# Kernel optimization log

Hardware: AMD Instinct MI355X
Metric: run time of the kernel (lower is better)

The kernel has to match this reference:

```python
import jax, jax.numpy as jnp
import numpy as np

BS, V, H, W = 2, 4, 24, 24
C, K, L, NH = 256, 16, 6, 8
DH = C // NH
FF = 4 * C
EPS = 1e-5


def _ln(x, w, b):
    m = jnp.mean(x, axis=-1, keepdims=True)
    v = jnp.mean((x - m) ** 2, axis=-1, keepdims=True)
    return (x - m) * jax.lax.rsqrt(v + EPS) * w + b


def _pe(x, W1, b1, W2, b2):
    # PositionEmbeddingLearnedMLP: Linear(3,C) -> ReLU -> Linear(C,C), channels-last
    return jax.nn.relu(x @ W1.T + b1) @ W2.T + b2


def setup_inputs():
    key = jax.random.key(0)
    ks = jax.random.split(key, 8)
    s = 0.02
    return {
        "feature": jax.random.normal(ks[0], (BS * V, C, H, W), jnp.float32),
        "xyz": jax.random.uniform(ks[1], (BS * V, H, W, 3), jnp.float32),
        "pe_W1": jax.random.normal(ks[2], (C, 3), jnp.float32) * s,
        "pe_b1": jnp.zeros((C,), jnp.float32),
        "pe_W2": jax.random.normal(ks[3], (C, C), jnp.float32) * s,
        "pe_b2": jnp.zeros((C,), jnp.float32),
        "Wqkv": jax.random.normal(ks[4], (L, 3 * C, C), jnp.float32) * s,
        "bqkv": jnp.zeros((L, 3 * C), jnp.float32),
        "Wo": jax.random.normal(ks[5], (L, C, C), jnp.float32) * s,
        "bo": jnp.zeros((L, C), jnp.float32),
        "ln_attn_w": jnp.ones((L, C), jnp.float32),
        "ln_attn_b": jnp.zeros((L, C), jnp.float32),
        "W1": jax.random.normal(ks[6], (L, FF, C), jnp.float32) * s,
        "b1": jnp.zeros((L, FF), jnp.float32),
        "W2": jax.random.normal(ks[7], (L, C, FF), jnp.float32) * s,
        "b2": jnp.zeros((L, C), jnp.float32),
        "ln_ffn_w": jnp.ones((L, C), jnp.float32),
        "ln_ffn_b": jnp.zeros((L, C), jnp.float32),
        "ln_out_w": jnp.ones((L, C), jnp.float32),
        "ln_out_b": jnp.zeros((L, C), jnp.float32),
    }


def _forward(feature, xyz, pe_W1, pe_b1, pe_W2, pe_b2, Wqkv, bqkv, Wo, bo,
             ln_attn_w, ln_attn_b, W1, b1, W2, b2, ln_ffn_w, ln_ffn_b,
             ln_out_w, ln_out_b):
    N = V * H * W
    # (B*V,C,H,W) -> (BS,N,C) ; (B*V,H,W,3) -> (BS,N,3) : flatten views+pixels
    feat = feature.reshape(BS, V, C, H, W).transpose(0, 1, 3, 4, 2).reshape(BS, N, C)
    pts = xyz.reshape(BS, N, 3)
    # per-batch KNN (self included), mirroring pointops.queryandgroup
    d2 = jnp.sum((pts[:, :, None, :] - pts[:, None, :, :]) ** 2, axis=-1)  # (BS,N,N)
    _, idx = jax.lax.top_k(-d2, K)  # (BS,N,K) nearest-neighbor indices
    grouped = jax.vmap(lambda p, i: p[i])(pts, idx)  # (BS,N,K,3)
    rel = grouped - pts[:, :, None, :]  # relative coords (use_xyz=True)
    q_pe = _pe(jnp.zeros((3,), feat.dtype), pe_W1, pe_b1, pe_W2, pe_b2)  # (C,)
    k_pe = _pe(rel, pe_W1, pe_b1, pe_W2, pe_b2).reshape(BS * N, K, C)
    idx_g = (idx + (jnp.arange(BS) * N)[:, None, None]).reshape(BS * N, K)
    out = feat.reshape(BS * N, C)
    for i in range(L):
        keyf = out[idx_g]  # (BN,K,C) per-layer neighbor gather
        # CrossAttentionLayer, pre-norm
        t2 = _ln(out, ln_attn_w[i], ln_attn_b[i])
        q = (t2 + q_pe) @ Wqkv[i, :C].T + bqkv[i, :C]
        k = (keyf + k_pe) @ Wqkv[i, C:2 * C].T + bqkv[i, C:2 * C]
        v = keyf @ Wqkv[i, 2 * C:].T + bqkv[i, 2 * C:]
        qh = q.reshape(-1, NH, DH)
        kh = k.reshape(-1, K, NH, DH)
        vh = v.reshape(-1, K, NH, DH)
        att = jax.nn.softmax(jnp.einsum('bhd,bkhd->bhk', qh, kh) * (DH ** -0.5), axis=-1)
        ao = jnp.einsum('bhk,bkhd->bhd', att, vh).reshape(-1, C) @ Wo[i].T + bo[i]
        out = out + ao
        # FFNLayer, pre-norm
        t2 = _ln(out, ln_ffn_w[i], ln_ffn_b[i])
        out = out + (jax.nn.relu(t2 @ W1[i].T + b1[i]) @ W2[i].T + b2[i])
        # extra per-layer LayerNorm
        out = _ln(out, ln_out_w[i], ln_out_b[i])
    return out.reshape(BS, V, H, W, C).transpose(0, 1, 4, 2, 3).reshape(BS * V, C, H, W)


def reference(feature, xyz, pe_W1, pe_b1, pe_W2, pe_b2, Wqkv, bqkv, Wo, bo,
              ln_attn_w, ln_attn_b, W1, b1, W2, b2, ln_ffn_w, ln_ffn_b,
              ln_out_w, ln_out_b):
    return _forward(feature, xyz, pe_W1, pe_b1, pe_W2, pe_b2, Wqkv, bqkv, Wo, bo,
                    ln_attn_w, ln_attn_b, W1, b1, W2, b2, ln_ffn_w, ln_ffn_b,
                    ln_out_w, ln_out_b)
```

## Files before the change

### kernel.cpp

```cpp
#include <hip/hip_runtime.h>
#include <math.h>

#define BS_ 2
#define V_ 4
#define H_ 24
#define W_ 24
#define N_ (V_*H_*W_)
#define BN_ (BS_*N_)
#define C_ 256
#define K_ 16
#define L_ 6
#define NH_ 8
#define DH_ 32
#define FF_ 1024

typedef __attribute__((ext_vector_type(4))) float f32x4;
typedef __attribute__((ext_vector_type(8))) short bf16x8;
typedef __attribute__((ext_vector_type(4))) unsigned u32x4;

__device__ inline unsigned short f2bf(float x) {
    unsigned u = __float_as_uint(x);
    unsigned r = u + 0x7fffu + ((u >> 16) & 1u);
    return (unsigned short)(r >> 16);
}
__device__ inline float bf2f(unsigned short h) {
    return __uint_as_float(((unsigned)h) << 16);
}

__global__ __launch_bounds__(256) void f2bf5_kernel(const float* __restrict__ s0,
                                                    const float* __restrict__ s1,
                                                    const float* __restrict__ s2,
                                                    const float* __restrict__ s3,
                                                    const float* __restrict__ s4,
                                                    unsigned short* __restrict__ dst) {
    const int c0 = 65536, c1 = 1245184, c2 = 1638400, c3 = 3211264, c4 = 4784128;
    int i = blockIdx.x*256 + threadIdx.x;
    if (i >= c4) return;
    float v;
    if (i < c0)      v = s0[i];
    else if (i < c1) v = s1[i - c0];
    else if (i < c2) v = s2[i - c1];
    else if (i < c3) v = s3[i - c2];
    else             v = s4[i - c3];
    dst[i] = f2bf(v);
}

__global__ __launch_bounds__(256) void reshape_in_ln(const float* __restrict__ f,
                                                     const float* __restrict__ lnw,
                                                     const float* __restrict__ lnb,
                                                     const float* __restrict__ qpe,
                                                     float* __restrict__ w_out,
                                                     unsigned short* __restrict__ b_out,
                                                     unsigned short* __restrict__ b_t2) {
    int bn = blockIdx.x, c = threadIdx.x;
    int b = bn / N_, rem = bn % N_;
    int v = rem / (H_*W_), hw = rem % (H_*W_);
    float x = f[(((size_t)(b*V_ + v)*C_ + c)*(H_*W_)) + hw];
    w_out[(size_t)bn*C_ + c] = x;
    b_out[(size_t)bn*C_ + c] = f2bf(x);
    __shared__ float red[4];
    float s = x;
    #pragma unroll
    for (int off = 32; off; off >>= 1) s += __shfl_xor(s, off, 64);
    if ((c & 63) == 0) red[c >> 6] = s;
    __syncthreads();
    float mean = (red[0]+red[1]+red[2]+red[3]) * (1.f/C_);
    __syncthreads();
    float dx = x - mean;
    s = dx*dx;
    #pragma unroll
    for (int off = 32; off; off >>= 1) s += __shfl_xor(s, off, 64);
    if ((c & 63) == 0) red[c >> 6] = s;
    __syncthreads();
    float var = (red[0]+red[1]+red[2]+red[3]) * (1.f/C_);
    float y = dx * rsqrtf(var + 1e-5f) * lnw[c] + lnb[c] + qpe[c];
    b_t2[(size_t)bn*C_ + c] = f2bf(y);
}

__global__ __launch_bounds__(256) void reshape_out_kernel(const float* __restrict__ in,
                                                          float* __restrict__ o) {
    int bn = blockIdx.x, c = threadIdx.x;
    int b = bn / N_, rem = bn % N_;
    int v = rem / (H_*W_), hw = rem % (H_*W_);
    o[(((size_t)(b*V_ + v)*C_ + c)*(H_*W_)) + hw] = in[(size_t)bn*C_ + c];
}

__global__ __launch_bounds__(256) void knn_kernel(const float* __restrict__ pts,
                                                  int* __restrict__ idx) {
    int wid = threadIdx.x >> 6, lane = threadIdx.x & 63;
    int point = blockIdx.x*4 + wid;
    int b = point / N_;
    int il = point % N_;
    __shared__ float ps[N_*3];
    for (int l = threadIdx.x; l < N_*3; l += 256) ps[l] = pts[(size_t)b*N_*3 + l];
    __syncthreads();
    float qx = ps[il*3], qy = ps[il*3+1], qz = ps[il*3+2];
    unsigned long long key[36];
    #pragma unroll
    for (int s = 0; s < 36; ++s) {
        int j = lane + 64*s;
        float dx = qx - ps[j*3], dy = qy - ps[j*3+1], dz = qz - ps[j*3+2];
        float d2 = dx*dx + dy*dy + dz*dz;
        key[s] = ((unsigned long long)__float_as_uint(d2) << 32) | (unsigned)j;
    }
    for (int it = 0; it < K_; ++it) {
        unsigned long long b0 = key[0], b1 = key[1], b2 = key[2], b3 = key[3];
        #pragma unroll
        for (int s = 4; s < 36; s += 4) {
            b0 = key[s]   < b0 ? key[s]   : b0;
            b1 = key[s+1] < b1 ? key[s+1] : b1;
            b2 = key[s+2] < b2 ? key[s+2] : b2;
            b3 = key[s+3] < b3 ? key[s+3] : b3;
        }
        unsigned long long m01 = b0 < b1 ? b0 : b1;
        unsigned long long m23 = b2 < b3 ? b2 : b3;
        unsigned long long best = m01 < m23 ? m01 : m23;
        #pragma unroll
        for (int off = 32; off; off >>= 1) {
            unsigned long long o = __shfl_xor(best, off, 64);
            if (o < best) best = o;
        }
        int wj = (int)(best & 0xffffffffu);
        if (lane == 0) idx[point*K_ + it] = b*N_ + wj;
        if ((wj & 63) == lane) {
            int sw = wj >> 6;
            #pragma unroll
            for (int s = 0; s < 36; ++s) if (s == sw) key[s] = ~0ull;
        }
    }
}

__global__ __launch_bounds__(256) void qpe_kernel(const float* __restrict__ b1,
                                                  const float* __restrict__ W2,
                                                  const float* __restrict__ b2,
                                                  float* __restrict__ qpe) {
    __shared__ float h[C_];
    int tid = threadIdx.x;
    h[tid] = fmaxf(b1[tid], 0.f);
    __syncthreads();
    float acc = 0.f;
    for (int j = 0; j < C_; ++j) acc += h[j] * W2[(size_t)tid*C_ + j];
    qpe[tid] = acc + b2[tid];
}

__global__ __launch_bounds__(256) void kpe_kernel(const float* __restrict__ pts,
                                                  const int* __restrict__ idx,
                                                  const float* __restrict__ W1,
                                                  const float* __restrict__ b1,
                                                  const unsigned short* __restrict__ Wpe,
                                                  const float* __restrict__ pb2,
                                                  unsigned short* __restrict__ kpe) {
    int tid = threadIdx.x;
    int wave = tid >> 6, lane = tid & 63;
    int wr = wave >> 1, wc = wave & 1;
    int n0 = blockIdx.x * 64;
    int m0 = blockIdx.y * 64;
    __shared__ float relS[64][4];
    __shared__ float w1S[256][4];
    __shared__ unsigned short hid[64][264];
    __shared__ unsigned short Ws[2][64][40];
    w1S[tid][0] = W1[tid*3+0];
    w1S[tid][1] = W1[tid*3+1];
    w1S[tid][2] = W1[tid*3+2];
    w1S[tid][3] = b1[tid];
    if (tid < 64) {
        int row = m0 + tid;
        int p = row >> 4;
        int j = idx[row];
        relS[tid][0] = pts[(size_t)j*3+0] - pts[(size_t)p*3+0];
        relS[tid][1] = pts[(size_t)j*3+1] - pts[(size_t)p*3+1];
        relS[tid][2] = pts[(size_t)j*3+2] - pts[(size_t)p*3+2];
    }
    int rw = tid >> 2, ch = tid & 3;
    const unsigned short* pW = Wpe + (size_t)(n0 + rw)*C_ + ch*8;
    *(bf16x8*)&Ws[0][rw][ch*8] = *(const bf16x8*)pW;
    __syncthreads();
    {
        int r = tid >> 2, cq = (tid & 3) * 64;
        float r0 = relS[r][0], r1 = relS[r][1], r2 = relS[r][2];
        #pragma unroll
        for (int u8 = 0; u8 < 8; ++u8) {
            unsigned short tmp[8];
            #pragma unroll
            for (int v = 0; v < 8; ++v) {
                int c = cq + u8*8 + v;
                f32x4 w4 = *(const f32x4*)&w1S[c][0];
                float val = r0*w4[0] + r1*w4[1] + r2*w4[2] + w4[3];
                tmp[v] = f2bf(fmaxf(val, 0.f));
            }
            *(bf16x8*)&hid[r][cq + u8*8] = *(bf16x8*)tmp;
        }
    }
    __syncthreads();
    f32x4 acc[2][2];
    #pragma unroll
    for (int i = 0; i < 2; ++i)
        #pragma unroll
        for (int j = 0; j < 2; ++j) acc[i][j] = (f32x4){0.f,0.f,0.f,0.f};
    for (int t = 0; t < 8; ++t) {
        int cur = t & 1;
        bool nx = (t < 7);
        bf16x8 lw;
        if (nx) lw = *(const bf16x8*)(pW + (t+1)*32);
        int kf = (lane >> 4) * 8;
        bf16x8 af[2], wf[2];
        #pragma unroll
        for (int i = 0; i < 2; ++i) af[i] = *(const bf16x8*)&hid[wr*32 + i*16 + (lane & 15)][t*32 + kf];
        #pragma unroll
        for (int j = 0; j < 2; ++j) wf[j] = *(const bf16x8*)&Ws[cur][wc*32 + j*16 + (lane & 15)][kf];
        #pragma unroll
        for (int i = 0; i < 2; ++i)
            #pragma unroll
            for (int j = 0; j < 2; ++j)
                acc[i][j] = __builtin_amdgcn_mfma_f32_16x16x32_bf16(af[i], wf[j], acc[i][j], 0, 0, 0);
        if (nx) *(bf16x8*)&Ws[cur^1][rw][ch*8] = lw;
        __syncthreads();
    }
    #pragma unroll
    for (int i = 0; i < 2; ++i)
        #pragma unroll
        for (int j = 0; j < 2; ++j)
            #pragma unroll
            for (int rg = 0; rg < 4; ++rg) {
                int mr = m0 + wr*32 + i*16 + (lane >> 4)*4 + rg;
                int col = n0 + wc*32 + j*16 + (lane & 15);
                kpe[(size_t)mr*C_ + col] = f2bf(acc[i][j][rg] + pb2[col]);
            }
}

template<int ACT, bool RES, int OMODE>
__device__ __forceinline__ void gemm_body(const unsigned short* __restrict__ A, int sA,
                                          const unsigned short* __restrict__ W, int sW,
                                          const float* __restrict__ bias, int bcol0,
                                          const float* __restrict__ res,
                                          float* __restrict__ outF,
                                          unsigned short* __restrict__ outB,
                                          int sO, int on0, int m0, int K) {
    __shared__ unsigned short As[2][64][40];
    __shared__ unsigned short Ws[2][64][40];
    int tid = threadIdx.x;
    int wave = tid >> 6, lane = tid & 63;
    int wr = wave >> 1, wc = wave & 1;
    f32x4 acc[2][2];
    #pragma unroll
    for (int i = 0; i < 2; ++i)
        #pragma unroll
        for (int j = 0; j < 2; ++j) acc[i][j] = (f32x4){0.f, 0.f, 0.f, 0.f};

    int r = tid >> 2, ch = tid & 3;
    const unsigned short* pA = A + (size_t)(m0 + r)*sA + ch*8;
    const unsigned short* pW = W + (size_t)r*sW + ch*8;
    *(bf16x8*)&As[0][r][ch*8] = *(const bf16x8*)pA;
    *(bf16x8*)&Ws[0][r][ch*8] = *(const bf16x8*)pW;
    __syncthreads();
    int nk = K >> 5;
    for (int t = 0; t < nk; ++t) {
        int cur = t & 1;
        bool has_next = (t + 1 < nk);
        bf16x8 la, lw;
        if (has_next) {
            la = *(const bf16x8*)(pA + (t+1)*32);
            lw = *(const bf16x8*)(pW + (t+1)*32);
        }
        int kf = (lane >> 4) * 8;
        bf16x8 af[2], wf[2];
        #pragma unroll
        for (int i = 0; i < 2; ++i) af[i] = *(const bf16x8*)&As[cur][wr*32 + i*16 + (lane & 15)][kf];
        #pragma unroll
        for (int j = 0; j < 2; ++j) wf[j] = *(const bf16x8*)&Ws[cur][wc*32 + j*16 + (lane & 15)][kf];
        #pragma unroll
        for (int i = 0; i < 2; ++i)
            #pragma unroll
            for (int j = 0; j < 2; ++j)
                acc[i][j] = __builtin_amdgcn_mfma_f32_16x16x32_bf16(af[i], wf[j], acc[i][j], 0, 0, 0);
        if (has_next) {
            *(bf16x8*)&As[cur^1][r][ch*8] = la;
            *(bf16x8*)&Ws[cur^1][r][ch*8] = lw;
        }
        __syncthreads();
    }
    #pragma unroll
    for (int i = 0; i < 2; ++i) {
        #pragma unroll
        for (int j = 0; j < 2; ++j) {
            #pragma unroll
            for (int rg = 0; rg < 4; ++rg) {
                int m = m0 + wr*32 + i*16 + (lane >> 4)*4 + rg;
                int pl = wc*32 + j*16 + (lane & 15);
                float v = acc[i][j][rg];
                if (bias) v += bias[bcol0 + pl];
                if (ACT == 1) v = fmaxf(v, 0.f);
                if (RES) v += res[(size_t)m*sO + on0 + pl];
                if (OMODE != 2) outF[(size_t)m*sO + on0 + pl] = v;
                if (OMODE != 0) outB[(size_t)m*sO + on0 + pl] = f2bf(v);
            }
        }
    }
}

template<int ACT, bool RES, int OMODE>
__global__ __launch_bounds__(256) void gemm_k(const unsigned short* __restrict__ A,
                                              const unsigned short* __restrict__ W,
                                              const float* __restrict__ bias,
                                              const float* __restrict__ res,
                                              float* __restrict__ outF,
                                              unsigned short* __restrict__ outB,
                                              int P, int K) {
    int n0 = blockIdx.x * 64, m0 = blockIdx.y * 64;
    gemm_body<ACT,RES,OMODE>(A, K, W + (size_t)n0*K, K, bias, n0, res, outF, outB, P, n0, m0, K);
}

__global__ __launch_bounds__(256) void qkv_kernel(const unsigned short* __restrict__ t2,
                                                  const unsigned short* __restrict__ outb,
                                                  const unsigned short* __restrict__ Wqkv_l,
                                                  const float* __restrict__ bqkv_l,
                                                  unsigned short* __restrict__ b_q,
                                                  unsigned short* __restrict__ b_kv) {
    int bx = blockIdx.x;
    int n0 = bx * 64;
    int m0 = blockIdx.y * 64;
    if (bx < 4) {
        gemm_body<0,false,2>(t2, C_, Wqkv_l + (size_t)n0*C_, C_, bqkv_l, n0,
                             nullptr, nullptr, b_q, 256, n0, m0, C_);
    } else {
        gemm_body<0,false,2>(outb, C_, Wqkv_l + (size_t)n0*C_, C_, bqkv_l, n0,
                             nullptr, nullptr, b_kv, 512, n0 - 256, m0, C_);
    }
}

template<int VAR>
__global__ __launch_bounds__(256) void gemm_ln(const unsigned short* __restrict__ A,
                                               const unsigned short* __restrict__ W,
                                               const float* __restrict__ bias,
                                               const float* __restrict__ res,
                                               const float* __restrict__ lnw1, const float* __restrict__ lnb1,
                                               const float* __restrict__ lnw2, const float* __restrict__ lnb2,
                                               const float* __restrict__ qpe,
                                               float* __restrict__ outF,
                                               unsigned short* __restrict__ outB,
                                               unsigned short* __restrict__ outT2,
                                               int K) {
    __shared__ unsigned short Ws[2][256][40];
    __shared__ unsigned short As[2][16][40];
    int tid = threadIdx.x;
    int wave = tid >> 6, lane = tid & 63;
    int m0 = blockIdx.x * 16;
    f32x4 acc[4];
    #pragma unroll
    for (int j = 0; j < 4; ++j) acc[j] = (f32x4){0.f,0.f,0.f,0.f};
    int rw = tid >> 2, ch = tid & 3;
    const unsigned short* pW = W + (size_t)rw*K + ch*8;
    const unsigned short* pA = A + (size_t)(m0 + ((tid & 63) >> 2))*K + (tid & 3)*8;
    #pragma unroll
    for (int c = 0; c < 4; ++c)
        *(bf16x8*)&Ws[0][c*64 + rw][ch*8] = *(const bf16x8*)(pW + (size_t)c*64*K);
    if (tid < 64) *(bf16x8*)&As[0][tid >> 2][(tid & 3)*8] = *(const bf16x8*)pA;
    __syncthreads();
    int nk = K >> 5;
    for (int t = 0; t < nk; ++t) {
        int cur = t & 1;
        bool nx = (t + 1 < nk);
        bf16x8 lw0, lw1, lw2, lw3, la;
        if (nx) {
            lw0 = *(const bf16x8*)(pW + (size_t)0*64*K + (t+1)*32);
            lw1 = *(const bf16x8*)(pW + (size_t)1*64*K + (t+1)*32);
            lw2 = *(const bf16x8*)(pW + (size_t)2*64*K + (t+1)*32);
            lw3 = *(const bf16x8*)(pW + (size_t)3*64*K + (t+1)*32);
            if (tid < 64) la = *(const bf16x8*)(pA + (t+1)*32);
        }
        int kf = (lane >> 4) * 8;
        bf16x8 af = *(const bf16x8*)&As[cur][lane & 15][kf];
        #pragma unroll
        for (int j = 0; j < 4; ++j) {
            bf16x8 wf = *(const bf16x8*)&Ws[cur][wave*64 + j*16 + (lane & 15)][kf];
            acc[j] = __builtin_amdgcn_mfma_f32_16x16x32_bf16(af, wf, acc[j], 0, 0, 0);
        }
        if (nx) {
            *(bf16x8*)&Ws[cur^1][0*64 + rw][ch*8] = lw0;
            *(bf16x8*)&Ws[cur^1][1*64 + rw][ch*8] = lw1;
            *(bf16x8*)&Ws[cur^1][2*64 + rw][ch*8] = lw2;
            *(bf16x8*)&Ws[cur^1][3*64 + rw][ch*8] = lw3;
            if (tid < 64) *(bf16x8*)&As[cur^1][tid >> 2][(tid & 3)*8] = la;
        }
        __syncthreads();
    }
    float* S = (float*)&Ws[0][0][0];
    #pragma unroll
    for (int j = 0; j < 4; ++j) {
        int col = wave*64 + j*16 + (lane & 15);
        #pragma unroll
        for (int rg = 0; rg < 4; ++rg) {
            int row = (lane >> 4)*4 + rg;
            S[row*260 + col] = acc[j][rg] + bias[col] + res[(size_t)(m0+row)*C_ + col];
        }
    }
    __syncthreads();
    int row = tid >> 4, g = tid & 15;
    size_t m = m0 + row;
    float x[16];
    #pragma unroll
    for (int u = 0; u < 4; ++u) {
        f32x4 v4 = *(const f32x4*)&S[row*260 + g*16 + u*4];
        x[u*4+0] = v4[0]; x[u*4+1] = v4[1]; x[u*4+2] = v4[2]; x[u*4+3] = v4[3];
    }
    float s1 = 0.f, s2 = 0.f;
    #pragma unroll
    for (int u = 0; u < 16; ++u) { s1 += x[u]; s2 += x[u]*x[u]; }
    #pragma unroll
    for (int off = 8; off; off >>= 1) { s1 += __shfl_xor(s1, off, 16); s2 += __shfl_xor(s2, off, 16); }
    float mean = s1 * (1.f/C_);
    float var  = s2 * (1.f/C_) - mean*mean;
    float rstd = rsqrtf(var + 1e-5f);
    float y1[16];
    #pragma unroll
    for (int u = 0; u < 4; ++u) {
        f32x4 w4 = *(const f32x4*)&lnw1[g*16 + u*4];
        f32x4 b4 = *(const f32x4*)&lnb1[g*16 + u*4];
        #pragma unroll
        for (int v = 0; v < 4; ++v)
            y1[u*4+v] = (x[u*4+v] - mean)*rstd*w4[v] + b4[v];
    }
    if (VAR == 0) {
        #pragma unroll
        for (int u = 0; u < 4; ++u) {
            f32x4 v4 = { x[u*4], x[u*4+1], x[u*4+2], x[u*4+3] };
            *(f32x4*)&outF[m*C_ + g*16 + u*4] = v4;
        }
        unsigned pk[8];
        #pragma unroll
        for (int u = 0; u < 8; ++u) pk[u] = (unsigned)f2bf(y1[2*u]) | ((unsigned)f2bf(y1[2*u+1]) << 16);
        *(u32x4*)&outT2[m*C_ + g*16]     = *(u32x4*)&pk[0];
        *(u32x4*)&outT2[m*C_ + g*16 + 8] = *(u32x4*)&pk[4];
    } else {
        #pragma unroll
        for (int u = 0; u < 4; ++u) {
            f32x4 v4 = { y1[u*4], y1[u*4+1], y1[u*4+2], y1[u*4+3] };
            *(f32x4*)&outF[m*C_ + g*16 + u*4] = v4;
        }
        if (VAR == 1) {
            unsigned pk[8];
            #pragma unroll
            for (int u = 0; u < 8; ++u) pk[u] = (unsigned)f2bf(y1[2*u]) | ((unsigned)f2bf(y1[2*u+1]) << 16);
            *(u32x4*)&outB[m*C_ + g*16]     = *(u32x4*)&pk[0];
            *(u32x4*)&outB[m*C_ + g*16 + 8] = *(u32x4*)&pk[4];
            float t1 = 0.f, t2s = 0.f;
            #pragma unroll
            for (int u = 0; u < 16; ++u) { t1 += y1[u]; t2s += y1[u]*y1[u]; }
            #pragma unroll
            for (int off = 8; off; off >>= 1) { t1 += __shfl_xor(t1, off, 16); t2s += __shfl_xor(t2s, off, 16); }
            float mean2 = t1 * (1.f/C_);
            float var2  = t2s * (1.f/C_) - mean2*mean2;
            float rstd2 = rsqrtf(var2 + 1e-5f);
            unsigned pk2[8];
            #pragma unroll
            for (int u = 0; u < 4; ++u) {
                f32x4 w4 = *(const f32x4*)&lnw2[g*16 + u*4];
                f32x4 b4 = *(const f32x4*)&lnb2[g*16 + u*4];
                f32x4 q4 = *(const f32x4*)&qpe[g*16 + u*4];
                float z0 = (y1[u*4+0]-mean2)*rstd2*w4[0] + b4[0] + q4[0];
                float z1 = (y1[u*4+1]-mean2)*rstd2*w4[1] + b4[1] + q4[1];
                float z2 = (y1[u*4+2]-mean2)*rstd2*w4[2] + b4[2] + q4[2];
                float z3 = (y1[u*4+3]-mean2)*rstd2*w4[3] + b4[3] + q4[3];
                pk2[u*2]   = (unsigned)f2bf(z0) | ((unsigned)f2bf(z1) << 16);
                pk2[u*2+1] = (unsigned)f2bf(z2) | ((unsigned)f2bf(z3) << 16);
            }
            *(u32x4*)&outT2[m*C_ + g*16]     = *(u32x4*)&pk2[0];
            *(u32x4*)&outT2[m*C_ + g*16 + 8] = *(u32x4*)&pk2[4];
        }
    }
}

__global__ __launch_bounds__(256) void rk_kernel(const unsigned short* __restrict__ q,
                                                 const unsigned short* __restrict__ Wqkv_l,
                                                 unsigned short* __restrict__ r) {
    int n0 = blockIdx.x * 64, m0 = blockIdx.y * 64, h = blockIdx.z;
    __shared__ unsigned short As[64][40];
    __shared__ unsigned short Ws[64][40];
    int tid = threadIdx.x;
    int wave = tid >> 6, lane = tid & 63;
    int wr = wave >> 1, wc = wave & 1;
    *(bf16x8*)&As[tid>>2][(tid&3)*8] =
        *(const bf16x8*)&q[(size_t)(m0 + (tid>>2))*C_ + h*DH_ + (tid&3)*8];
    {
        int d = tid >> 3, cg = tid & 7;
        bf16x8 wv = *(const bf16x8*)&Wqkv_l[(size_t)(C_ + h*DH_ + d)*C_ + n0 + cg*8];
        #pragma unroll
        for (int j = 0; j < 8; ++j) Ws[cg*8 + j][d] = (unsigned short)wv[j];
    }
    __syncthreads();
    int kf = (lane >> 4) * 8;
    bf16x8 af[2], wf[2];
    #pragma unroll
    for (int i = 0; i < 2; ++i) af[i] = *(const bf16x8*)&As[wr*32 + i*16 + (lane & 15)][kf];
    #pragma unroll
    for (int j = 0; j < 2; ++j) wf[j] = *(const bf16x8*)&Ws[wc*32 + j*16 + (lane & 15)][kf];
    f32x4 acc[2][2];
    #pragma unroll
    for (int i = 0; i < 2; ++i)
        #pragma unroll
        for (int j = 0; j < 2; ++j)
            acc[i][j] = __builtin_amdgcn_mfma_f32_16x16x32_bf16(af[i], wf[j],
                          (f32x4){0.f,0.f,0.f,0.f}, 0, 0, 0);
    #pragma unroll
    for (int i = 0; i < 2; ++i)
        #pragma unroll
        for (int j = 0; j < 2; ++j)
            #pragma unroll
            for (int rg = 0; rg < 4; ++rg) {
                int m = m0 + wr*32 + i*16 + (lane >> 4)*4 + rg;
                int pl = wc*32 + j*16 + (lane & 15);
                r[(size_t)m*(NH_*C_) + h*C_ + n0 + pl] = f2bf(acc[i][j][rg]);
            }
}

__global__ __launch_bounds__(256) void attn_kernel(const unsigned short* __restrict__ q,
                                                   const unsigned short* __restrict__ kv,
                                                   const unsigned short* __restrict__ kpe,
                                                   const unsigned short* __restrict__ r,
                                                   const int* __restrict__ idx,
                                                   unsigned short* __restrict__ ao) {
    int wid = threadIdx.x >> 6, lane = threadIdx.x & 63;
    int point = blockIdx.x*4 + wid;
    __shared__ __align__(16) unsigned short vs[4][K_][264];
    __shared__ __align__(16) float atts[4][NH_][K_];
    int row = lane & 15;
    int off8 = (lane >> 4) * 8;
    int idx_l = idx[point*K_ + row];

    #pragma unroll
    for (int t = 0; t < 8; ++t) {
        int vr = 2*t + (lane >> 5);
        int j = __shfl(idx_l, vr, 64);
        int cc = (lane & 31) * 8;
        *(bf16x8*)&vs[wid][vr][cc] = *(const bf16x8*)&kv[(size_t)j*512 + 256 + cc];
    }

    f32x4 acc = {0.f, 0.f, 0.f, 0.f};
    const bf16x8 zero8 = {0,0,0,0,0,0,0,0};
    #pragma unroll
    for (int s = 0; s < 8; ++s) {
        bf16x8 a = *(const bf16x8*)&kpe[((size_t)point*K_ + row)*C_ + s*32 + off8];
        bf16x8 b = zero8;
        if (row < 8) b = *(const bf16x8*)&r[(size_t)point*NH_*C_ + row*C_ + s*32 + off8];
        acc = __builtin_amdgcn_mfma_f32_16x16x32_bf16(a, b, acc, 0, 0, 0);
    }
    #pragma unroll
    for (int s = 0; s < 8; ++s) {
        bf16x8 a = *(const bf16x8*)&kv[(size_t)idx_l*512 + s*32 + off8];
        bf16x8 b = zero8;
        if (row == 8 + s) b = *(const bf16x8*)&q[(size_t)point*C_ + s*32 + off8];
        acc = __builtin_amdgcn_mfma_f32_16x16x32_bf16(a, b, acc, 0, 0, 0);
    }

    const float scale = 0.1767766952966369f;
    float sv[4], m = -1e30f;
    #pragma unroll
    for (int rg = 0; rg < 4; ++rg) {
        float o = __shfl_xor(acc[rg], 8, 64);
        sv[rg] = (acc[rg] + o) * scale;
        m = fmaxf(m, sv[rg]);
    }
    m = fmaxf(m, __shfl_xor(m, 16, 64));
    m = fmaxf(m, __shfl_xor(m, 32, 64));
    float sum = 0.f;
    #pragma unroll
    for (int rg = 0; rg < 4; ++rg) { sv[rg] = __expf(sv[rg] - m); sum += sv[rg]; }
    sum += __shfl_xor(sum, 16, 64);
    sum += __shfl_xor(sum, 32, 64);
    float inv = 1.f / sum;
    if (row < 8) {
        f32x4 av = { sv[0]*inv, sv[1]*inv, sv[2]*inv, sv[3]*inv };
        *(f32x4*)&atts[wid][row][(lane >> 4) * 4] = av;
    }

    int h = lane >> 3;
    float att_f[16];
    #pragma unroll
    for (int u = 0; u < 4; ++u) {
        f32x4 t4 = *(const f32x4*)&atts[wid][h][u*4];
        att_f[u*4+0] = t4[0]; att_f[u*4+1] = t4[1]; att_f[u*4+2] = t4[2]; att_f[u*4+3] = t4[3];
    }
    int cbase = lane * 4;
    float o0 = 0.f, o1 = 0.f, o2 = 0.f, o3 = 0.f;
    #pragma unroll
    for (int k = 0; k < K_; ++k) {
        unsigned long long vv = *(const unsigned long long*)&vs[wid][k][cbase];
        unsigned lo = (unsigned)vv, hi = (unsigned)(vv >> 32);
        float a = att_f[k];
        o0 += a * __uint_as_float(lo << 16);
        o1 += a * __uint_as_float(lo & 0xffff0000u);
        o2 += a * __uint_as_float(hi << 16);
        o3 += a * __uint_as_float(hi & 0xffff0000u);
    }
    unsigned p0 = (unsigned)f2bf(o0) | ((unsigned)f2bf(o1) << 16);
    unsigned p1 = (unsigned)f2bf(o2) | ((unsigned)f2bf(o3) << 16);
    unsigned out2[2] = { p0, p1 };
    *(unsigned long long*)&ao[(size_t)point*C_ + cbase] = *(const unsigned long long*)out2;
}

extern "C" void kernel_launch(void* const* d_in, const int* in_sizes, int n_in,
                              void* d_out, int out_size, void* d_ws, size_t ws_size,
                              hipStream_t stream) {
    const float* feature  = (const float*)d_in[0];
    const float* xyz      = (const float*)d_in[1];
    const float* pe_W1    = (const float*)d_in[2];
    const float* pe_b1    = (const float*)d_in[3];
    const float* pe_W2    = (const float*)d_in[4];
    const float* pe_b2    = (const float*)d_in[5];
    const float* Wqkv     = (const float*)d_in[6];
    const float* bqkv     = (const float*)d_in[7];
    const float* Wo       = (const float*)d_in[8];
    const float* bo       = (const float*)d_in[9];
    const float* ln_attn_w= (const float*)d_in[10];
    const float* ln_attn_b= (const float*)d_in[11];
    const float* W1       = (const float*)d_in[12];
    const float* b1       = (const float*)d_in[13];
    const float* W2       = (const float*)d_in[14];
    const float* b2       = (const float*)d_in[15];
    const float* ln_ffn_w = (const float*)d_in[16];
    const float* ln_ffn_b = (const float*)d_in[17];
    const float* ln_out_w = (const float*)d_in[18];
    const float* ln_out_b = (const float*)d_in[19];

    float* ws = (float*)d_ws;
    float* w_out = ws;
    float* w_qpe = w_out + (size_t)BN_*C_;
    unsigned short* bptr = (unsigned short*)(w_qpe + C_ + 64);
    unsigned short* b_out = bptr;  bptr += (size_t)BN_*C_;
    unsigned short* b_t2  = bptr;  bptr += (size_t)BN_*C_;
    unsigned short* b_q   = bptr;  bptr += (size_t)BN_*C_;
    unsigned short* b_kv  = bptr;  bptr += (size_t)BN_*512;
    unsigned short* b_ao  = bptr;  bptr += (size_t)BN_*C_;
    unsigned short* b_ffh = bptr;  bptr += (size_t)BN_*FF_;
    unsigned short* w_kpe = bptr;  bptr += (size_t)BN_*K_*C_;
    unsigned short* w_r   = bptr;  bptr += (size_t)BN_*NH_*C_;
    unsigned short* bWpe  = bptr;  bptr += (size_t)C_*C_;
    unsigned short* bWqkv = bptr;  bptr += (size_t)L_*3*C_*C_;
    unsigned short* bWo   = bptr;  bptr += (size_t)L_*C_*C_;
    unsigned short* bW1   = bptr;  bptr += (size_t)L_*FF_*C_;
    unsigned short* bW2   = bptr;  bptr += (size_t)L_*C_*FF_;
    int* w_idx = (int*)bptr;

    f2bf5_kernel<<<(4784128 + 255)/256, 256, 0, stream>>>(pe_W2, Wqkv, Wo, W1, W2, bWpe);
    knn_kernel<<<BN_/4, 256, 0, stream>>>(xyz, w_idx);
    qpe_kernel<<<1, 256, 0, stream>>>(pe_b1, pe_W2, pe_b2, w_qpe);
    reshape_in_ln<<<BN_, 256, 0, stream>>>(feature, ln_attn_w, ln_attn_b, w_qpe,
                                           w_out, b_out, b_t2);
    kpe_kernel<<<dim3(C_/64, (BN_*K_)/64), 256, 0, stream>>>(xyz, w_idx, pe_W1, pe_b1,
                                                             bWpe, pe_b2, w_kpe);

    for (int i = 0; i < L_; ++i) {
        const unsigned short* Wqkv_l = bWqkv + (size_t)i*3*C_*C_;
        const float* bqkv_l = bqkv + (size_t)i*3*C_;

        qkv_kernel<<<dim3(12, BN_/64), 256, 0, stream>>>(b_t2, b_out, Wqkv_l, bqkv_l, b_q, b_kv);
        rk_kernel<<<dim3(4, BN_/64, NH_), 256, 0, stream>>>(b_q, Wqkv_l, w_r);
        attn_kernel<<<BN_/4, 256, 0, stream>>>(b_q, b_kv, w_kpe, w_r, w_idx, b_ao);
        gemm_ln<0><<<BN_/16, 256, 0, stream>>>(
            b_ao, bWo + (size_t)i*C_*C_, bo + i*C_, w_out,
            ln_ffn_w + i*C_, ln_ffn_b + i*C_, nullptr, nullptr, nullptr,
            w_out, nullptr, b_t2, C_);
        gemm_k<1,false,2><<<dim3(FF_/64, BN_/64), 256, 0, stream>>>(
            b_t2, bW1 + (size_t)i*FF_*C_, b1 + i*FF_, nullptr, nullptr, b_ffh, FF_, C_);
        if (i < L_-1) {
            gemm_ln<1><<<BN_/16, 256, 0, stream>>>(
                b_ffh, bW2 + (size_t)i*C_*FF_, b2 + i*C_, w_out,
                ln_out_w + i*C_, ln_out_b + i*C_,
                ln_attn_w + (i+1)*C_, ln_attn_b + (i+1)*C_, w_qpe,
                w_out, b_out, b_t2, FF_);
        } else {
            gemm_ln<2><<<BN_/16, 256, 0, stream>>>(
                b_ffh, bW2 + (size_t)i*C_*FF_, b2 + i*C_, w_out,
                ln_out_w + i*C_, ln_out_b + i*C_, nullptr, nullptr, nullptr,
                w_out, nullptr, nullptr, FF_);
        }
    }

    reshape_out_kernel<<<BN_, 256, 0, stream>>>(w_out, (float*)d_out);
}
```

Measured before the change: 682.6 us.

## Pre-swizzle weights into MFMA fragment layout and load B operands directly to registers

Adds a weight conversion kernel that writes bf16 weights in per-lane MFMA fragment order, so the GEMM kernels load B fragments straight from global memory into registers instead of staging them through shared memory. Both the tiled GEMM and the GEMM+LayerNorm kernels drop their weight LDS buffers and the matching stores. The key positional-embedding kernel is split into a hidden-layer kernel that writes a large bf16 intermediate plus a generic GEMM. The trade-offs are extra conversion launches each call, an extra global round trip for the PE hidden activations, and a plain bf16 copy of Wqkv still kept for rk_kernel.

```diff
diff --git a/kernel.cpp b/kernel.cpp
--- a/kernel.cpp
+++ b/kernel.cpp
@@ -27,22 +27,24 @@
     return __uint_as_float(((unsigned)h) << 16);
 }
 
-__global__ __launch_bounds__(256) void f2bf5_kernel(const float* __restrict__ s0,
-                                                    const float* __restrict__ s1,
-                                                    const float* __restrict__ s2,
-                                                    const float* __restrict__ s3,
-                                                    const float* __restrict__ s4,
-                                                    unsigned short* __restrict__ dst) {
-    const int c0 = 65536, c1 = 1245184, c2 = 1638400, c3 = 3211264, c4 = 4784128;
+__global__ __launch_bounds__(256) void f2bf_kernel(const float* __restrict__ in,
+                                                   unsigned short* __restrict__ out, int n) {
     int i = blockIdx.x*256 + threadIdx.x;
-    if (i >= c4) return;
-    float v;
-    if (i < c0)      v = s0[i];
-    else if (i < c1) v = s1[i - c0];
-    else if (i < c2) v = s2[i - c1];
-    else if (i < c3) v = s3[i - c2];
-    else             v = s4[i - c3];
-    dst[i] = f2bf(v);
+    if (i < n) out[i] = f2bf(in[i]);
+}
+
+__global__ __launch_bounds__(256) void w2frag_kernel(const float* __restrict__ W,
+                                                     unsigned short* __restrict__ F,
+                                                     int P, int K) {
+    int wid = threadIdx.x >> 6, lane = threadIdx.x & 63;
+    int tile = blockIdx.x*4 + wid;
+    int nkt = K >> 5;
+    int tn = tile / nkt, tk = tile - tn*nkt;
+    const float* src = W + (size_t)(tn*16 + (lane & 15))*K + tk*32 + (lane >> 4)*8;
+    unsigned short tmp[8];
+    #pragma unroll
+    for (int j = 0; j < 8; ++j) tmp[j] = f2bf(src[j]);
+    *(bf16x8*)&F[(size_t)tile*512 + lane*8] = *(bf16x8*)tmp;
 }
 
 __global__ __launch_bounds__(256) void reshape_in_ln(const float* __restrict__ f,
@@ -143,104 +145,41 @@
     qpe[tid] = acc + b2[tid];
 }
 
-__global__ __launch_bounds__(256) void kpe_kernel(const float* __restrict__ pts,
-                                                  const int* __restrict__ idx,
-                                                  const float* __restrict__ W1,
-                                                  const float* __restrict__ b1,
-                                                  const unsigned short* __restrict__ Wpe,
-                                                  const float* __restrict__ pb2,
-                                                  unsigned short* __restrict__ kpe) {
+__global__ __launch_bounds__(256) void pe_hidden_kernel(const float* __restrict__ pts,
+                                                        const int* __restrict__ idx,
+                                                        const float* __restrict__ W1,
+                                                        const float* __restrict__ b1,
+                                                        unsigned short* __restrict__ hidden) {
+    int point = blockIdx.x;
+    int c = threadIdx.x;
+    __shared__ float rel[K_][3];
+    if (threadIdx.x < K_*3) {
+        int k = threadIdx.x / 3, ax = threadIdx.x % 3;
+        int j = idx[point*K_ + k];
+        rel[k][ax] = pts[(size_t)j*3 + ax] - pts[(size_t)point*3 + ax];
+    }
+    __syncthreads();
+    float w0 = W1[c*3], w1 = W1[c*3+1], w2 = W1[c*3+2], bb = b1[c];
+    #pragma unroll
+    for (int k = 0; k < K_; ++k) {
+        float v = rel[k][0]*w0 + rel[k][1]*w1 + rel[k][2]*w2 + bb;
+        hidden[((size_t)point*K_ + k)*C_ + c] = f2bf(fmaxf(v, 0.f));
+    }
+}
+
+template<int ACT, bool RES, int OMODE>
+__device__ __forceinline__ void gemm_body2(const unsigned short* __restrict__ A, int sA,
+                                           const unsigned short* __restrict__ Wf,
+                                           const float* __restrict__ bias, int bcol0,
+                                           const float* __restrict__ res,
+                                           float* __restrict__ outF,
+                                           unsigned short* __restrict__ outB,
+                                           int sO, int on0, int m0, int K) {
+    __shared__ unsigned short As[2][64][40];
     int tid = threadIdx.x;
     int wave = tid >> 6, lane = tid & 63;
     int wr = wave >> 1, wc = wave & 1;
-    int n0 = blockIdx.x * 64;
-    int m0 = blockIdx.y * 64;
-    __shared__ float relS[64][4];
-    __shared__ float w1S[256][4];
-    __shared__ unsigned short hid[64][264];
-    __shared__ unsigned short Ws[2][64][40];
-    w1S[tid][0] = W1[tid*3+0];
-    w1S[tid][1] = W1[tid*3+1];
-    w1S[tid][2] = W1[tid*3+2];
-    w1S[tid][3] = b1[tid];
-    if (tid < 64) {
-        int row = m0 + tid;
-        int p = row >> 4;
-        int j = idx[row];
-        relS[tid][0] = pts[(size_t)j*3+0] - pts[(size_t)p*3+0];
-        relS[tid][1] = pts[(size_t)j*3+1] - pts[(size_t)p*3+1];
-        relS[tid][2] = pts[(size_t)j*3+2] - pts[(size_t)p*3+2];
-    }
-    int rw = tid >> 2, ch = tid & 3;
-    const unsigned short* pW = Wpe + (size_t)(n0 + rw)*C_ + ch*8;
-    *(bf16x8*)&Ws[0][rw][ch*8] = *(const bf16x8*)pW;
-    __syncthreads();
-    {
-        int r = tid >> 2, cq = (tid & 3) * 64;
-        float r0 = relS[r][0], r1 = relS[r][1], r2 = relS[r][2];
-        #pragma unroll
-        for (int u8 = 0; u8 < 8; ++u8) {
-            unsigned short tmp[8];
-            #pragma unroll
-            for (int v = 0; v < 8; ++v) {
-                int c = cq + u8*8 + v;
-                f32x4 w4 = *(const f32x4*)&w1S[c][0];
-                float val = r0*w4[0] + r1*w4[1] + r2*w4[2] + w4[3];
-                tmp[v] = f2bf(fmaxf(val, 0.f));
-            }
-            *(bf16x8*)&hid[r][cq + u8*8] = *(bf16x8*)tmp;
-        }
-    }
-    __syncthreads();
-    f32x4 acc[2][2];
-    #pragma unroll
-    for (int i = 0; i < 2; ++i)
-        #pragma unroll
-        for (int j = 0; j < 2; ++j) acc[i][j] = (f32x4){0.f,0.f,0.f,0.f};
-    for (int t = 0; t < 8; ++t) {
-        int cur = t & 1;
-        bool nx = (t < 7);
-        bf16x8 lw;
-        if (nx) lw = *(const bf16x8*)(pW + (t+1)*32);
-        int kf = (lane >> 4) * 8;
-        bf16x8 af[2], wf[2];
-        #pragma unroll
-        for (int i = 0; i < 2; ++i) af[i] = *(const bf16x8*)&hid[wr*32 + i*16 + (lane & 15)][t*32 + kf];
-        #pragma unroll
-        for (int j = 0; j < 2; ++j) wf[j] = *(const bf16x8*)&Ws[cur][wc*32 + j*16 + (lane & 15)][kf];
-        #pragma unroll
-        for (int i = 0; i < 2; ++i)
-            #pragma unroll
-            for (int j = 0; j < 2; ++j)
-                acc[i][j] = __builtin_amdgcn_mfma_f32_16x16x32_bf16(af[i], wf[j], acc[i][j], 0, 0, 0);
-        if (nx) *(bf16x8*)&Ws[cur^1][rw][ch*8] = lw;
-        __syncthreads();
-    }
-    #pragma unroll
-    for (int i = 0; i < 2; ++i)
-        #pragma unroll
-        for (int j = 0; j < 2; ++j)
-            #pragma unroll
-            for (int rg = 0; rg < 4; ++rg) {
-                int mr = m0 + wr*32 + i*16 + (lane >> 4)*4 + rg;
-                int col = n0 + wc*32 + j*16 + (lane & 15);
-                kpe[(size_t)mr*C_ + col] = f2bf(acc[i][j][rg] + pb2[col]);
-            }
-}
-
-template<int ACT, bool RES, int OMODE>
-__device__ __forceinline__ void gemm_body(const unsigned short* __restrict__ A, int sA,
-                                          const unsigned short* __restrict__ W, int sW,
-                                          const float* __restrict__ bias, int bcol0,
-                                          const float* __restrict__ res,
-                                          float* __restrict__ outF,
-                                          unsigned short* __restrict__ outB,
-                                          int sO, int on0, int m0, int K) {
-    __shared__ unsigned short As[2][64][40];
-    __shared__ unsigned short Ws[2][64][40];
-    int tid = threadIdx.x;
-    int wave = tid >> 6, lane = tid & 63;
-    int wr = wave >> 1, wc = wave & 1;
+    int nkt = K >> 5;
     f32x4 acc[2][2];
     #pragma unroll
     for (int i = 0; i < 2; ++i)
@@ -249,34 +188,29 @@
 
     int r = tid >> 2, ch = tid & 3;
     const unsigned short* pA = A + (size_t)(m0 + r)*sA + ch*8;
-    const unsigned short* pW = W + (size_t)r*sW + ch*8;
+    const unsigned short* bb = Wf + (size_t)(wc*2)*nkt*512 + lane*8;
     *(bf16x8*)&As[0][r][ch*8] = *(const bf16x8*)pA;
-    *(bf16x8*)&Ws[0][r][ch*8] = *(const bf16x8*)pW;
-    __syncthreads();
-    int nk = K >> 5;
-    for (int t = 0; t < nk; ++t) {
+    bf16x8 bw0 = *(const bf16x8*)bb;
+    bf16x8 bw1 = *(const bf16x8*)(bb + (size_t)nkt*512);
+    __syncthreads();
+    for (int t = 0; t < nkt; ++t) {
         int cur = t & 1;
-        bool has_next = (t + 1 < nk);
-        bf16x8 la, lw;
-        if (has_next) {
-            la = *(const bf16x8*)(pA + (t+1)*32);
-            lw = *(const bf16x8*)(pW + (t+1)*32);
+        bool nx = (t + 1 < nkt);
+        bf16x8 la, nb0, nb1;
+        if (nx) {
+            la  = *(const bf16x8*)(pA + (t+1)*32);
+            nb0 = *(const bf16x8*)(bb + (size_t)(t+1)*512);
+            nb1 = *(const bf16x8*)(bb + (size_t)nkt*512 + (size_t)(t+1)*512);
         }
         int kf = (lane >> 4) * 8;
-        bf16x8 af[2], wf[2];
-        #pragma unroll
-        for (int i = 0; i < 2; ++i) af[i] = *(const bf16x8*)&As[cur][wr*32 + i*16 + (lane & 15)][kf];
-        #pragma unroll
-        for (int j = 0; j < 2; ++j) wf[j] = *(const bf16x8*)&Ws[cur][wc*32 + j*16 + (lane & 15)][kf];
-        #pragma unroll
-        for (int i = 0; i < 2; ++i)
-            #pragma unroll
-            for (int j = 0; j < 2; ++j)
-                acc[i][j] = __builtin_amdgcn_mfma_f32_16x16x32_bf16(af[i], wf[j], acc[i][j], 0, 0, 0);
-        if (has_next) {
-            *(bf16x8*)&As[cur^1][r][ch*8] = la;
-            *(bf16x8*)&Ws[cur^1][r][ch*8] = lw;
-        }
+        bf16x8 af0 = *(const bf16x8*)&As[cur][wr*32 + (lane & 15)][kf];
+        bf16x8 af1 = *(const bf16x8*)&As[cur][wr*32 + 16 + (lane & 15)][kf];
+        acc[0][0] = __builtin_amdgcn_mfma_f32_16x16x32_bf16(af0, bw0, acc[0][0], 0, 0, 0);
+        acc[0][1] = __builtin_amdgcn_mfma_f32_16x16x32_bf16(af0, bw1, acc[0][1], 0, 0, 0);
+        acc[1][0] = __builtin_amdgcn_mfma_f32_16x16x32_bf16(af1, bw0, acc[1][0], 0, 0, 0);
+        acc[1][1] = __builtin_amdgcn_mfma_f32_16x16x32_bf16(af1, bw1, acc[1][1], 0, 0, 0);
+        if (nx) *(bf16x8*)&As[cur^1][r][ch*8] = la;
+        bw0 = nb0; bw1 = nb1;
         __syncthreads();
     }
     #pragma unroll
@@ -299,99 +233,92 @@
 }
 
 template<int ACT, bool RES, int OMODE>
-__global__ __launch_bounds__(256) void gemm_k(const unsigned short* __restrict__ A,
-                                              const unsigned short* __restrict__ W,
-                                              const float* __restrict__ bias,
-                                              const float* __restrict__ res,
-                                              float* __restrict__ outF,
-                                              unsigned short* __restrict__ outB,
-                                              int P, int K) {
-    int n0 = blockIdx.x * 64, m0 = blockIdx.y * 64;
-    gemm_body<ACT,RES,OMODE>(A, K, W + (size_t)n0*K, K, bias, n0, res, outF, outB, P, n0, m0, K);
-}
-
-__global__ __launch_bounds__(256) void qkv_kernel(const unsigned short* __restrict__ t2,
-                                                  const unsigned short* __restrict__ outb,
-                                                  const unsigned short* __restrict__ Wqkv_l,
-                                                  const float* __restrict__ bqkv_l,
-                                                  unsigned short* __restrict__ b_q,
-                                                  unsigned short* __restrict__ b_kv) {
-    int bx = blockIdx.x;
-    int n0 = bx * 64;
-    int m0 = blockIdx.y * 64;
-    if (bx < 4) {
-        gemm_body<0,false,2>(t2, C_, Wqkv_l + (size_t)n0*C_, C_, bqkv_l, n0,
-                             nullptr, nullptr, b_q, 256, n0, m0, C_);
-    } else {
-        gemm_body<0,false,2>(outb, C_, Wqkv_l + (size_t)n0*C_, C_, bqkv_l, n0,
-                             nullptr, nullptr, b_kv, 512, n0 - 256, m0, C_);
-    }
-}
-
-template<int VAR>
-__global__ __launch_bounds__(256) void gemm_ln(const unsigned short* __restrict__ A,
-                                               const unsigned short* __restrict__ W,
+__global__ __launch_bounds__(256) void gemm_k2(const unsigned short* __restrict__ A,
+                                               const unsigned short* __restrict__ Wf0,
                                                const float* __restrict__ bias,
                                                const float* __restrict__ res,
-                                               const float* __restrict__ lnw1, const float* __restrict__ lnb1,
-                                               const float* __restrict__ lnw2, const float* __restrict__ lnb2,
-                                               const float* __restrict__ qpe,
                                                float* __restrict__ outF,
                                                unsigned short* __restrict__ outB,
-                                               unsigned short* __restrict__ outT2,
-                                               int K) {
-    __shared__ unsigned short Ws[2][256][40];
+                                               int P, int K) {
+    int n0 = blockIdx.x * 64, m0 = blockIdx.y * 64;
+    const unsigned short* Wf = Wf0 + (size_t)(n0 >> 4)*(K >> 5)*512;
+    gemm_body2<ACT,RES,OMODE>(A, K, Wf, bias, n0, res, outF, outB, P, n0, m0, K);
+}
+
+__global__ __launch_bounds__(256) void qkv_kernel2(const unsigned short* __restrict__ t2,
+                                                   const unsigned short* __restrict__ outb,
+                                                   const unsigned short* __restrict__ Fqkv_l,
+                                                   const float* __restrict__ bqkv_l,
+                                                   unsigned short* __restrict__ b_q,
+                                                   unsigned short* __restrict__ b_kv) {
+    int bx = blockIdx.x;
+    int m0 = blockIdx.y * 64;
+    const unsigned short* Wf = Fqkv_l + (size_t)(bx*4)*8*512;
+    if (bx < 4) {
+        gemm_body2<0,false,2>(t2, C_, Wf, bqkv_l, bx*64, nullptr, nullptr, b_q, 256, bx*64, m0, C_);
+    } else {
+        gemm_body2<0,false,2>(outb, C_, Wf, bqkv_l, bx*64, nullptr, nullptr, b_kv, 512, bx*64 - 256, m0, C_);
+    }
+}
+
+template<int VAR>
+__global__ __launch_bounds__(256) void gemm_ln2(const unsigned short* __restrict__ A,
+                                                const unsigned short* __restrict__ Wf,
+                                                const float* __restrict__ bias,
+                                                const float* __restrict__ res,
+                                                const float* __restrict__ lnw1, const float* __restrict__ lnb1,
+                                                const float* __restrict__ lnw2, const float* __restrict__ lnb2,
+                                                const float* __restrict__ qpe,
+                                                float* __restrict__ outF,
+                                                unsigned short* __restrict__ outB,
+                                                unsigned short* __restrict__ outT2,
+                                                int K) {
     __shared__ unsigned short As[2][16][40];
+    __shared__ float S[16][260];
     int tid = threadIdx.x;
     int wave = tid >> 6, lane = tid & 63;
     int m0 = blockIdx.x * 16;
+    int nkt = K >> 5;
     f32x4 acc[4];
     #pragma unroll
     for (int j = 0; j < 4; ++j) acc[j] = (f32x4){0.f,0.f,0.f,0.f};
-    int rw = tid >> 2, ch = tid & 3;
-    const unsigned short* pW = W + (size_t)rw*K + ch*8;
     const unsigned short* pA = A + (size_t)(m0 + ((tid & 63) >> 2))*K + (tid & 3)*8;
-    #pragma unroll
-    for (int c = 0; c < 4; ++c)
-        *(bf16x8*)&Ws[0][c*64 + rw][ch*8] = *(const bf16x8*)(pW + (size_t)c*64*K);
+    const unsigned short* bb = Wf + (size_t)(wave*4)*nkt*512 + lane*8;
     if (tid < 64) *(bf16x8*)&As[0][tid >> 2][(tid & 3)*8] = *(const bf16x8*)pA;
-    __syncthreads();
-    int nk = K >> 5;
-    for (int t = 0; t < nk; ++t) {
+    bf16x8 bw[4];
+    #pragma unroll
+    for (int j = 0; j < 4; ++j) bw[j] = *(const bf16x8*)(bb + (size_t)j*nkt*512);
+    __syncthreads();
+    for (int t = 0; t < nkt; ++t) {
         int cur = t & 1;
-        bool nx = (t + 1 < nk);
-        bf16x8 lw0, lw1, lw2, lw3, la;
+        bool nx = (t + 1 < nkt);
+        bf16x8 la, nb0, nb1, nb2, nb3;
         if (nx) {
-            lw0 = *(const bf16x8*)(pW + (size_t)0*64*K + (t+1)*32);
-            lw1 = *(const bf16x8*)(pW + (size_t)1*64*K + (t+1)*32);
-            lw2 = *(const bf16x8*)(pW + (size_t)2*64*K + (t+1)*32);
-            lw3 = *(const bf16x8*)(pW + (size_t)3*64*K + (t+1)*32);
+            nb0 = *(const bf16x8*)(bb + (size_t)0*nkt*512 + (size_t)(t+1)*512);
+            nb1 = *(const bf16x8*)(bb + (size_t)1*nkt*512 + (size_t)(t+1)*512);
+            nb2 = *(const bf16x8*)(bb + (size_t)2*nkt*512 + (size_t)(t+1)*512);
+            nb3 = *(const bf16x8*)(bb + (size_t)3*nkt*512 + (size_t)(t+1)*512);
             if (tid < 64) la = *(const bf16x8*)(pA + (t+1)*32);
         }
         int kf = (lane >> 4) * 8;
         bf16x8 af = *(const bf16x8*)&As[cur][lane & 15][kf];
-        #pragma unroll
-        for (int j = 0; j < 4; ++j) {
-            bf16x8 wf = *(const bf16x8*)&Ws[cur][wave*64 + j*16 + (lane & 15)][kf];
-            acc[j] = __builtin_amdgcn_mfma_f32_16x16x32_bf16(af, wf, acc[j], 0, 0, 0);
-        }
+        acc[0] = __builtin_amdgcn_mfma_f32_16x16x32_bf16(af, bw[0], acc[0], 0, 0, 0);
+        acc[1] = __builtin_amdgcn_mfma_f32_16x16x32_bf16(af, bw[1], acc[1], 0, 0, 0);
+        acc[2] = __builtin_amdgcn_mfma_f32_16x16x32_bf16(af, bw[2], acc[2], 0, 0, 0);
+        acc[3] = __builtin_amdgcn_mfma_f32_16x16x32_bf16(af, bw[3], acc[3], 0, 0, 0);
         if (nx) {
-            *(bf16x8*)&Ws[cur^1][0*64 + rw][ch*8] = lw0;
-            *(bf16x8*)&Ws[cur^1][1*64 + rw][ch*8] = lw1;
-            *(bf16x8*)&Ws[cur^1][2*64 + rw][ch*8] = lw2;
-            *(bf16x8*)&Ws[cur^1][3*64 + rw][ch*8] = lw3;
             if (tid < 64) *(bf16x8*)&As[cur^1][tid >> 2][(tid & 3)*8] = la;
+            bw[0] = nb0; bw[1] = nb1; bw[2] = nb2; bw[3] = nb3;
         }
         __syncthreads();
     }
-    float* S = (float*)&Ws[0][0][0];
     #pragma unroll
     for (int j = 0; j < 4; ++j) {
         int col = wave*64 + j*16 + (lane & 15);
         #pragma unroll
         for (int rg = 0; rg < 4; ++rg) {
             int row = (lane >> 4)*4 + rg;
-            S[row*260 + col] = acc[j][rg] + bias[col] + res[(size_t)(m0+row)*C_ + col];
+            S[row][col] = acc[j][rg] + bias[col] + res[(size_t)(m0+row)*C_ + col];
         }
     }
     __syncthreads();
@@ -400,7 +327,7 @@
     float x[16];
     #pragma unroll
     for (int u = 0; u < 4; ++u) {
-        f32x4 v4 = *(const f32x4*)&S[row*260 + g*16 + u*4];
+        f32x4 v4 = *(const f32x4*)&S[row][g*16 + u*4];
         x[u*4+0] = v4[0]; x[u*4+1] = v4[1]; x[u*4+2] = v4[2]; x[u*4+3] = v4[3];
     }
     float s1 = 0.f, s2 = 0.f;
@@ -634,43 +561,52 @@
     unsigned short* b_ffh = bptr;  bptr += (size_t)BN_*FF_;
     unsigned short* w_kpe = bptr;  bptr += (size_t)BN_*K_*C_;
     unsigned short* w_r   = bptr;  bptr += (size_t)BN_*NH_*C_;
-    unsigned short* bWpe  = bptr;  bptr += (size_t)C_*C_;
+    unsigned short* b_hid = bptr;  bptr += (size_t)BN_*K_*C_;
     unsigned short* bWqkv = bptr;  bptr += (size_t)L_*3*C_*C_;
-    unsigned short* bWo   = bptr;  bptr += (size_t)L_*C_*C_;
-    unsigned short* bW1   = bptr;  bptr += (size_t)L_*FF_*C_;
-    unsigned short* bW2   = bptr;  bptr += (size_t)L_*C_*FF_;
+    unsigned short* Fqkv  = bptr;  bptr += (size_t)L_*3*C_*C_;
+    unsigned short* Fo    = bptr;  bptr += (size_t)L_*C_*C_;
+    unsigned short* F1    = bptr;  bptr += (size_t)L_*FF_*C_;
+    unsigned short* F2    = bptr;  bptr += (size_t)L_*C_*FF_;
+    unsigned short* Fpe   = bptr;  bptr += (size_t)C_*C_;
     int* w_idx = (int*)bptr;
 
-    f2bf5_kernel<<<(4784128 + 255)/256, 256, 0, stream>>>(pe_W2, Wqkv, Wo, W1, W2, bWpe);
+    f2bf_kernel<<<(L_*3*C_*C_+255)/256, 256, 0, stream>>>(Wqkv, bWqkv, L_*3*C_*C_);
+    w2frag_kernel<<<(L_*3*C_*C_/512)/4, 256, 0, stream>>>(Wqkv, Fqkv, L_*3*C_, C_);
+    w2frag_kernel<<<(L_*C_*C_/512)/4,   256, 0, stream>>>(Wo,   Fo,   L_*C_,   C_);
+    w2frag_kernel<<<(L_*FF_*C_/512)/4,  256, 0, stream>>>(W1,   F1,   L_*FF_,  C_);
+    w2frag_kernel<<<(L_*C_*FF_/512)/4,  256, 0, stream>>>(W2,   F2,   L_*C_,   FF_);
+    w2frag_kernel<<<(C_*C_/512)/4,      256, 0, stream>>>(pe_W2, Fpe, C_,      C_);
+
     knn_kernel<<<BN_/4, 256, 0, stream>>>(xyz, w_idx);
     qpe_kernel<<<1, 256, 0, stream>>>(pe_b1, pe_W2, pe_b2, w_qpe);
     reshape_in_ln<<<BN_, 256, 0, stream>>>(feature, ln_attn_w, ln_attn_b, w_qpe,
                                            w_out, b_out, b_t2);
-    kpe_kernel<<<dim3(C_/64, (BN_*K_)/64), 256, 0, stream>>>(xyz, w_idx, pe_W1, pe_b1,
-                                                             bWpe, pe_b2, w_kpe);
+    pe_hidden_kernel<<<BN_, 256, 0, stream>>>(xyz, w_idx, pe_W1, pe_b1, b_hid);
+    gemm_k2<0,false,2><<<dim3(C_/64, (BN_*K_)/64), 256, 0, stream>>>(
+        b_hid, Fpe, pe_b2, nullptr, nullptr, w_kpe, C_, C_);
 
     for (int i = 0; i < L_; ++i) {
-        const unsigned short* Wqkv_l = bWqkv + (size_t)i*3*C_*C_;
+        const unsigned short* Fqkv_l = Fqkv + (size_t)i*3*C_*C_;
         const float* bqkv_l = bqkv + (size_t)i*3*C_;
 
-        qkv_kernel<<<dim3(12, BN_/64), 256, 0, stream>>>(b_t2, b_out, Wqkv_l, bqkv_l, b_q, b_kv);
-        rk_kernel<<<dim3(4, BN_/64, NH_), 256, 0, stream>>>(b_q, Wqkv_l, w_r);
+        qkv_kernel2<<<dim3(12, BN_/64), 256, 0, stream>>>(b_t2, b_out, Fqkv_l, bqkv_l, b_q, b_kv);
+        rk_kernel<<<dim3(4, BN_/64, NH_), 256, 0, stream>>>(b_q, bWqkv + (size_t)i*3*C_*C_, w_r);
         attn_kernel<<<BN_/4, 256, 0, stream>>>(b_q, b_kv, w_kpe, w_r, w_idx, b_ao);
-        gemm_ln<0><<<BN_/16, 256, 0, stream>>>(
-            b_ao, bWo + (size_t)i*C_*C_, bo + i*C_, w_out,
+        gemm_ln2<0><<<BN_/16, 256, 0, stream>>>(
+            b_ao, Fo + (size_t)i*C_*C_, bo + i*C_, w_out,
             ln_ffn_w + i*C_, ln_ffn_b + i*C_, nullptr, nullptr, nullptr,
             w_out, nullptr, b_t2, C_);
-        gemm_k<1,false,2><<<dim3(FF_/64, BN_/64), 256, 0, stream>>>(
-            b_t2, bW1 + (size_t)i*FF_*C_, b1 + i*FF_, nullptr, nullptr, b_ffh, FF_, C_);
+        gemm_k2<1,false,2><<<dim3(FF_/64, BN_/64), 256, 0, stream>>>(
+            b_t2, F1 + (size_t)i*FF_*C_, b1 + i*FF_, nullptr, nullptr, b_ffh, FF_, C_);
         if (i < L_-1) {
-            gemm_ln<1><<<BN_/16, 256, 0, stream>>>(
-                b_ffh, bW2 + (size_t)i*C_*FF_, b2 + i*C_, w_out,
+            gemm_ln2<1><<<BN_/16, 256, 0, stream>>>(
+                b_ffh, F2 + (size_t)i*C_*FF_, b2 + i*C_, w_out,
                 ln_out_w + i*C_, ln_out_b + i*C_,
                 ln_attn_w + (i+1)*C_, ln_attn_b + (i+1)*C_, w_qpe,
                 w_out, b_out, b_t2, FF_);
         } else {
-            gemm_ln<2><<<BN_/16, 256, 0, stream>>>(
-                b_ffh, bW2 + (size_t)i*C_*FF_, b2 + i*C_, w_out,
+            gemm_ln2<2><<<BN_/16, 256, 0, stream>>>(
+                b_ffh, F2 + (size_t)i*C_*FF_, b2 + i*C_, w_out,
                 ln_out_w + i*C_, ln_out_b + i*C_, nullptr, nullptr, nullptr,
                 w_out, nullptr, nullptr, FF_);
         }
```

After: 666.7 us. 2.3% less time.
